# Kernel optimization log

Measured on AMD Instinct MI355X. Metric: run time of the kernel, lower is better.

Reference implementation:

```python
import jax, jax.numpy as jnp
import numpy as np

D_MODEL = 1024

def setup_inputs() -> dict:
    key = jax.random.key(0)
    ks = jax.random.split(key, 7)
    B, S, D = 4, 2048, D_MODEL
    scale = 1.0 / np.sqrt(D)
    x = jax.random.normal(ks[0], (B, S, D), dtype=jnp.float32)
    Wq = jax.random.normal(ks[1], (D, D), dtype=jnp.float32) * scale
    bq = jnp.zeros((D,), dtype=jnp.float32)
    Wk = jax.random.normal(ks[2], (D, D), dtype=jnp.float32) * scale
    bk = jnp.zeros((D,), dtype=jnp.float32)
    Wv = jax.random.normal(ks[3], (D, D), dtype=jnp.float32) * scale
    bv = jnp.zeros((D,), dtype=jnp.float32)
    return {"x": x, "Wq": Wq, "bq": bq, "Wk": Wk, "bk": bk, "Wv": Wv, "bv": bv}

def reference(x, Wq, bq, Wk, bk, Wv, bv):
    # Single-head attention; scale = 1/sqrt(d_model) as in the torch module (self.d_k = d_model).
    d_k = x.shape[-1]
    q = jnp.einsum('bsd,de->bse', x, Wq) + bq
    k = jnp.einsum('bsd,de->bse', x, Wk) + bk
    v = jnp.einsum('bsd,de->bse', x, Wv) + bv
    scores = jnp.einsum('bqd,bkd->bqk', q, k) / jnp.sqrt(jnp.asarray(d_k, x.dtype))
    attn = jax.nn.softmax(scores, axis=-1)
    return jnp.einsum('bqk,bkd->bqd', attn, v)
```

## Files before the change

### kernel.cpp

```cpp
#include <hip/hip_runtime.h>
#include <hip/hip_bf16.h>

#define DM 1024
#define SEQ 2048
#define NBATCH 4

using f32x4 = __attribute__((ext_vector_type(4))) float;
using s16x8 = __attribute__((ext_vector_type(8))) short;
using u16x4 = __attribute__((ext_vector_type(4))) unsigned short;
using u16x8 = __attribute__((ext_vector_type(8))) unsigned short;

__device__ __forceinline__ unsigned short f2bf(float f) {
  union { float f; unsigned u; } v; v.f = f;
  return (unsigned short)((v.u + 0x7fffu + ((v.u >> 16) & 1u)) >> 16);
}

__global__ void prep_k(const float* __restrict__ X,
                       const float* __restrict__ Wq, const float* __restrict__ Wk,
                       const float* __restrict__ Wv,
                       unsigned short* __restrict__ XB, unsigned short* __restrict__ WT) {
  __shared__ float t[32][33];
  const int b = blockIdx.x;
  if (b < 4096) {
    const int i = b * 256 + threadIdx.x;
    const f32x4* p = (const f32x4*)X;
    f32x4 a = p[2 * i], c = p[2 * i + 1];
    u16x8 o;
#pragma unroll
    for (int q = 0; q < 4; q++) { o[q] = f2bf(a[q]); o[4 + q] = f2bf(c[q]); }
    *(u16x8*)(XB + (size_t)i * 8) = o;
  } else {
    const int r2 = b - 4096;
    const int seg = r2 >> 10;
    const int rem = r2 & 1023;
    const int k0 = (rem >> 5) * 32, n0 = (rem & 31) * 32;
    const float* W = (seg == 0) ? Wq : (seg == 1) ? Wk : Wv;
    unsigned short* out = WT + (size_t)seg * DM * DM;
    const int tr = threadIdx.x >> 5, tc = threadIdx.x & 31;
#pragma unroll
    for (int p = 0; p < 4; p++) {
      int r = tr + p * 8;
      t[r][tc] = W[(size_t)(k0 + r) * DM + n0 + tc];
    }
    __syncthreads();
#pragma unroll
    for (int p = 0; p < 4; p++) {
      int r = tr + p * 8;
      out[(size_t)(n0 + r) * DM + k0 + tc] = f2bf(t[tc][r]);
    }
  }
}

__global__ void combine_k(const float* __restrict__ ms, const float* __restrict__ ss,
                          float* __restrict__ T) {
  const int idx = blockIdx.x * 256 + threadIdx.x;
  const float* m = ms + (size_t)idx * 16;
  const float* s = ss + (size_t)idx * 32;
  float mv[16];
#pragma unroll
  for (int t = 0; t < 16; t++) mv[t] = m[t];
  float M = mv[0];
#pragma unroll
  for (int t = 1; t < 16; t++) M = fmaxf(M, mv[t]);
  float L = 0.f;
#pragma unroll
  for (int t = 0; t < 16; t++) L += (s[2 * t] + s[2 * t + 1]) * __expf(mv[t] - M);
  T[idx] = 1.0f;
#pragma unroll
  for (int t = 1; t < 16; t++) T[t * 8192 + idx] = __expf(mv[t - 1] - mv[t]);
  T[16 * 8192 + idx] = __expf(mv[15] - M) / L;
}

template <int MODE, int LDA, int LDB, int KDIM>
__global__ void gemm_nt(const unsigned short* __restrict__ A,
                        const unsigned short* __restrict__ B,
                        void* __restrict__ C0,
                        unsigned short* __restrict__ C1,
                        unsigned short* __restrict__ C2,
                        const float* __restrict__ bq,
                        const float* __restrict__ bk,
                        const float* __restrict__ bv,
                        float* __restrict__ sm,
                        float* __restrict__ sv,
                        const float* __restrict__ Tt) {
  __shared__ unsigned short lbuf[16384];
  unsigned short* lA = lbuf;
  unsigned short* lB = lbuf + 8192;

  const int tid = threadIdx.x;
  const int w = tid >> 6;
  const int L = tid & 63;
  const int wm = w & 1, wn = w >> 1;
  const int qd = L >> 4, ll = L & 15;

  const int bid = blockIdx.x;
  const int xcd = bid & 7, slot = bid >> 3;
  int bz, tileM, tileN, nT;
  if (MODE == 0) {
    const int pm = xcd & 3, pn = xcd >> 2;
    const int nloc = slot % 12, mloc = slot / 12;
    bz = 0; tileM = (pm * 16 + mloc) * 128; tileN = (pn * 12 + nloc) * 128; nT = 0;
  } else if (MODE == 1) {
    bz = xcd >> 1;
    const int mh = xcd & 1;
    const int nloc = slot & 15, mloc = slot >> 4;
    tileM = (mh * 8 + mloc) * 128; tileN = nloc * 128; nT = nloc;
  } else {
    bz = xcd >> 1;
    const int mh = xcd & 1;
    const int nloc = slot & 7, mloc = slot >> 3;
    tileM = (mh * 8 + mloc) * 128; tileN = nloc * 128; nT = nloc;
  }

  const unsigned short* Ab = A;
  const unsigned short* Bb = B;
  if (MODE == 1) { Ab += (size_t)bz * SEQ * DM; Bb += (size_t)bz * SEQ * DM; }
  if (MODE == 2) { Ab += (size_t)bz * SEQ * SEQ; Bb += (size_t)bz * DM * SEQ; }

  const int srow = tid >> 3;
  const int pch = tid & 7;
  const int gch = pch ^ (srow & 7);
  const unsigned short* gA = Ab + (size_t)(tileM + srow) * LDA + gch * 8;
  const unsigned short* gB = Bb + (size_t)(tileN + srow) * LDB + gch * 8;
  unsigned short* wA = &lA[srow * 64 + pch * 8];
  unsigned short* wB = &lB[srow * 64 + pch * 8];

  u16x8 rA[4], rB[4];
#define LOADT(kt) do {                                                         \
    const size_t kk_ = (size_t)(kt) * 64;                                      \
    _Pragma("unroll")                                                          \
    for (int i_ = 0; i_ < 4; i_++) {                                           \
      rA[i_] = *(const u16x8*)(gA + (size_t)i_ * 32 * LDA + kk_);              \
      rB[i_] = *(const u16x8*)(gB + (size_t)i_ * 32 * LDB + kk_);              \
    }                                                                          \
  } while (0)
#define WRITET() do {                                                          \
    _Pragma("unroll")                                                          \
    for (int i_ = 0; i_ < 4; i_++) {                                           \
      *(u16x8*)(wA + i_ * 32 * 64) = rA[i_];                                   \
      *(u16x8*)(wB + i_ * 32 * 64) = rB[i_];                                   \
    }                                                                          \
  } while (0)

  f32x4 acc[4][4];
#pragma unroll
  for (int i = 0; i < 4; i++)
#pragma unroll
    for (int j = 0; j < 4; j++) acc[i][j] = (f32x4){0.f, 0.f, 0.f, 0.f};

  const int sw = L & 7;

  float tTn[4][4];
  const float* Tb = nullptr;
  if (MODE == 2) {
    Tb = Tt + (size_t)bz * SEQ + tileM + wm * 64;
#pragma unroll
    for (int i = 0; i < 4; i++)
#pragma unroll
      for (int r = 0; r < 4; r++) tTn[i][r] = Tb[1 * 8192 + i * 16 + qd * 4 + r];
  }

  constexpr int NK = KDIM / 64;
  LOADT(0);
  WRITET();
  __syncthreads();

  for (int k = 0; k < NK; ++k) {
    if (MODE == 2 && k >= 2 && (k & 1) == 0) {
#pragma unroll
      for (int i = 0; i < 4; i++)
#pragma unroll
        for (int j = 0; j < 4; j++)
#pragma unroll
          for (int r = 0; r < 4; r++) acc[i][j][r] *= tTn[i][r];
      const int tn = (k >> 1) + 1;
#pragma unroll
      for (int i = 0; i < 4; i++)
#pragma unroll
        for (int r = 0; r < 4; r++) tTn[i][r] = Tb[(size_t)tn * 8192 + i * 16 + qd * 4 + r];
    }

    if (k + 1 < NK) LOADT(k + 1);

#pragma unroll
    for (int s = 0; s < 2; s++) {
      const int pc = ((s * 4 + qd) ^ sw) * 8;
      s16x8 av[4], bv4[4];
#pragma unroll
      for (int i = 0; i < 4; i++)
        av[i] = *(const s16x8*)&lA[(wm * 64 + i * 16 + ll) * 64 + pc];
#pragma unroll
      for (int j = 0; j < 4; j++)
        bv4[j] = *(const s16x8*)&lB[(wn * 64 + j * 16 + ll) * 64 + pc];
#pragma unroll
      for (int i = 0; i < 4; i++)
#pragma unroll
        for (int j = 0; j < 4; j++)
          acc[i][j] = __builtin_amdgcn_mfma_f32_16x16x32_bf16(av[i], bv4[j], acc[i][j], 0, 0, 0);
    }

    if (k + 1 < NK) {
      __builtin_amdgcn_s_waitcnt(0xC07F);
      __builtin_amdgcn_sched_barrier(0);
      __builtin_amdgcn_s_barrier();
      __builtin_amdgcn_sched_barrier(0);
      WRITET();
      __syncthreads();
    }
  }
#undef LOADT
#undef WRITET

  if (MODE == 0) {
#pragma unroll
    for (int i = 0; i < 4; i++) {
      const int gm0 = tileM + wm * 64 + i * 16 + qd * 4;
#pragma unroll
      for (int j = 0; j < 4; j++) {
        const int gn = tileN + wn * 64 + j * 16 + ll;
        const int seg = gn >> 10;
        const int colin = gn & 1023;
        if (seg == 0) {
          const float bias = bq[colin];
          unsigned short* Q = (unsigned short*)C0;
#pragma unroll
          for (int r = 0; r < 4; r++) Q[(size_t)(gm0 + r) * DM + colin] = f2bf(acc[i][j][r] + bias);
        } else if (seg == 1) {
          const float bias = bk[colin];
#pragma unroll
          for (int r = 0; r < 4; r++) C1[(size_t)(gm0 + r) * DM + colin] = f2bf(acc[i][j][r] + bias);
        } else {
          const float bias = bv[colin];
          u16x4 pk;
#pragma unroll
          for (int r = 0; r < 4; r++) pk[r] = f2bf(acc[i][j][r] + bias);
          const int b = gm0 >> 11, s0 = gm0 & 2047;
          *(u16x4*)(C2 + ((size_t)((b << 10) + colin)) * SEQ + s0) = pk;
        }
      }
    }
  } else if (MODE == 1) {
    __syncthreads();
    float mt[4][4];
#pragma unroll
    for (int i = 0; i < 4; i++)
#pragma unroll
      for (int r = 0; r < 4; r++) {
#pragma unroll
        for (int j = 0; j < 4; j++) acc[i][j][r] *= 0.03125f;
        float v = fmaxf(fmaxf(acc[i][0][r], acc[i][1][r]), fmaxf(acc[i][2][r], acc[i][3][r]));
#pragma unroll
        for (int m = 1; m < 16; m <<= 1) v = fmaxf(v, __shfl_xor(v, m, 16));
        mt[i][r] = v;
      }
    float* fred = (float*)lbuf;
    if (ll == 0) {
#pragma unroll
      for (int i = 0; i < 4; i++)
#pragma unroll
        for (int r = 0; r < 4; r++)
          fred[wn * 128 + wm * 64 + i * 16 + qd * 4 + r] = mt[i][r];
    }
    __syncthreads();
#pragma unroll
    for (int i = 0; i < 4; i++)
#pragma unroll
      for (int r = 0; r < 4; r++) {
        const int row = wm * 64 + i * 16 + qd * 4 + r;
        mt[i][r] = fmaxf(fred[row], fred[128 + row]);
      }
    __syncthreads();
#pragma unroll
    for (int i = 0; i < 4; i++)
#pragma unroll
      for (int r = 0; r < 4; r++) {
        const int row = wm * 64 + i * 16 + qd * 4 + r;
        float s = 0.f;
#pragma unroll
        for (int j = 0; j < 4; j++) {
          float e = __expf(acc[i][j][r] - mt[i][r]);
          s += e;
          const int col = wn * 64 + j * 16 + ll;
          lbuf[row * 128 + ((((col >> 4) ^ (row & 7)) << 4) | (col & 15))] = f2bf(e);
        }
#pragma unroll
        for (int m = 1; m < 16; m <<= 1) s += __shfl_xor(s, m, 16);
        if (ll == 0) {
          const size_t base = (size_t)bz * SEQ + tileM + row;
          sv[base * 32 + nT * 2 + wn] = s;
          if (wn == 0) sm[base * 16 + nT] = mt[i][r];
        }
      }
    __syncthreads();
    unsigned short* P = (unsigned short*)C0 + (size_t)bz * SEQ * SEQ;
#pragma unroll
    for (int p = 0; p < 8; p++) {
      const int c = p * 256 + tid;
      const int row = c >> 4, cg = c & 15;
      const int phys = ((((cg >> 1) ^ (row & 7)) << 4) | ((cg & 1) << 3));
      u16x8 val = *(const u16x8*)&lbuf[row * 128 + phys];
      *(u16x8*)(P + (size_t)(tileM + row) * SEQ + tileN + cg * 8) = val;
    }
  } else {
    float* O = (float*)C0 + (size_t)bz * SEQ * DM;
#pragma unroll
    for (int i = 0; i < 4; i++) {
      const int gm0 = tileM + wm * 64 + i * 16 + qd * 4;
#pragma unroll
      for (int j = 0; j < 4; j++) {
        const int gn = tileN + wn * 64 + j * 16 + ll;
#pragma unroll
        for (int r = 0; r < 4; r++)
          O[(size_t)(gm0 + r) * DM + gn] = acc[i][j][r] * tTn[i][r];
      }
    }
  }
}

extern "C" void kernel_launch(void* const* d_in, const int* in_sizes, int n_in,
                              void* d_out, int out_size, void* d_ws, size_t ws_size,
                              hipStream_t stream) {
  (void)in_sizes; (void)n_in; (void)out_size; (void)ws_size;
  const float* x  = (const float*)d_in[0];
  const float* Wq = (const float*)d_in[1];
  const float* bq = (const float*)d_in[2];
  const float* Wk = (const float*)d_in[3];
  const float* bk = (const float*)d_in[4];
  const float* Wv = (const float*)d_in[5];
  const float* bv = (const float*)d_in[6];
  float* out = (float*)d_out;
  char* ws = (char*)d_ws;
  unsigned short* xb = (unsigned short*)(ws + 0);
  unsigned short* wt = (unsigned short*)(ws + 16777216);
  unsigned short* qb = (unsigned short*)(ws + 23068672);
  unsigned short* kb = (unsigned short*)(ws + 39845888);
  unsigned short* vt = (unsigned short*)(ws + 56623104);
  unsigned short* P  = (unsigned short*)(ws + 73400320);
  float*          ms = (float*)(ws + 106954752);
  float*          ss = (float*)(ws + 107479040);
  float*          Tt = (float*)(ws + 108527616);

  prep_k<<<7168, 256, 0, stream>>>(x, Wq, Wk, Wv, xb, wt);
  gemm_nt<0, 1024, 1024, 1024><<<1536, 256, 0, stream>>>(
      xb, wt, (void*)qb, kb, vt, bq, bk, bv, nullptr, nullptr, nullptr);
  gemm_nt<1, 1024, 1024, 1024><<<1024, 256, 0, stream>>>(
      qb, kb, (void*)P, nullptr, nullptr, nullptr, nullptr, nullptr, ms, ss, nullptr);
  combine_k<<<32, 256, 0, stream>>>(ms, ss, Tt);
  gemm_nt<2, 2048, 2048, 2048><<<512, 256, 0, stream>>>(
      P, vt, (void*)out, nullptr, nullptr, nullptr, nullptr, nullptr, nullptr, nullptr, Tt);
}
```

Measured before the change: 273.1 us.

## Double-buffer LDS tiles in GEMM with one barrier per k-step

The GEMM kernel gets two LDS buffers instead of one, and global loads are prefetched two k-tiles ahead into registers. Each iteration writes the next tile into the idle buffer before computing on the current one. This replaces the two barriers per iteration (one before and one after the LDS write) with a single barrier. The cost is doubling shared memory per block to 64 KB, which may reduce how many blocks fit on a CU.

```diff
diff --git a/kernel.cpp b/kernel.cpp
--- a/kernel.cpp
+++ b/kernel.cpp
@@ -83,9 +83,7 @@
                         float* __restrict__ sm,
                         float* __restrict__ sv,
                         const float* __restrict__ Tt) {
-  __shared__ unsigned short lbuf[16384];
-  unsigned short* lA = lbuf;
-  unsigned short* lB = lbuf + 8192;
+  __shared__ unsigned short lbuf[32768];
 
   const int tid = threadIdx.x;
   const int w = tid >> 6;
@@ -122,8 +120,8 @@
   const int gch = pch ^ (srow & 7);
   const unsigned short* gA = Ab + (size_t)(tileM + srow) * LDA + gch * 8;
   const unsigned short* gB = Bb + (size_t)(tileN + srow) * LDB + gch * 8;
-  unsigned short* wA = &lA[srow * 64 + pch * 8];
-  unsigned short* wB = &lB[srow * 64 + pch * 8];
+  unsigned short* wA0 = &lbuf[srow * 64 + pch * 8];
+  unsigned short* wB0 = wA0 + 8192;
 
   u16x8 rA[4], rB[4];
 #define LOADT(kt) do {                                                         \
@@ -134,12 +132,20 @@
       rB[i_] = *(const u16x8*)(gB + (size_t)i_ * 32 * LDB + kk_);              \
     }                                                                          \
   } while (0)
-#define WRITET() do {                                                          \
+#define WRITET(b) do {                                                         \
+    unsigned short* wa_ = wA0 + (b) * 16384;                                   \
+    unsigned short* wb_ = wB0 + (b) * 16384;                                   \
     _Pragma("unroll")                                                          \
     for (int i_ = 0; i_ < 4; i_++) {                                           \
-      *(u16x8*)(wA + i_ * 32 * 64) = rA[i_];                                   \
-      *(u16x8*)(wB + i_ * 32 * 64) = rB[i_];                                   \
+      *(u16x8*)(wa_ + i_ * 32 * 64) = rA[i_];                                  \
+      *(u16x8*)(wb_ + i_ * 32 * 64) = rB[i_];                                  \
     }                                                                          \
+  } while (0)
+#define RAWBAR() do {                                                          \
+    __builtin_amdgcn_s_waitcnt(0xC07F);                   \
+    __builtin_amdgcn_sched_barrier(0);                                         \
+    __builtin_amdgcn_s_barrier();                                              \
+    __builtin_amdgcn_sched_barrier(0);                                         \
   } while (0)
 
   f32x4 acc[4][4];
@@ -162,10 +168,13 @@
 
   constexpr int NK = KDIM / 64;
   LOADT(0);
-  WRITET();
-  __syncthreads();
+  WRITET(0);
+  LOADT(1);
+  RAWBAR();
 
   for (int k = 0; k < NK; ++k) {
+    if (k + 1 < NK) WRITET((k + 1) & 1);
+
     if (MODE == 2 && k >= 2 && (k & 1) == 0) {
 #pragma unroll
       for (int i = 0; i < 4; i++)
@@ -180,18 +189,20 @@
         for (int r = 0; r < 4; r++) tTn[i][r] = Tb[(size_t)tn * 8192 + i * 16 + qd * 4 + r];
     }
 
-    if (k + 1 < NK) LOADT(k + 1);
-
+    if (k + 2 < NK) LOADT(k + 2);
+
+    const unsigned short* cA = lbuf + (k & 1) * 16384;
+    const unsigned short* cB = cA + 8192;
 #pragma unroll
     for (int s = 0; s < 2; s++) {
       const int pc = ((s * 4 + qd) ^ sw) * 8;
       s16x8 av[4], bv4[4];
 #pragma unroll
       for (int i = 0; i < 4; i++)
-        av[i] = *(const s16x8*)&lA[(wm * 64 + i * 16 + ll) * 64 + pc];
+        av[i] = *(const s16x8*)&cA[(wm * 64 + i * 16 + ll) * 64 + pc];
 #pragma unroll
       for (int j = 0; j < 4; j++)
-        bv4[j] = *(const s16x8*)&lB[(wn * 64 + j * 16 + ll) * 64 + pc];
+        bv4[j] = *(const s16x8*)&cB[(wn * 64 + j * 16 + ll) * 64 + pc];
 #pragma unroll
       for (int i = 0; i < 4; i++)
 #pragma unroll
@@ -199,17 +210,11 @@
           acc[i][j] = __builtin_amdgcn_mfma_f32_16x16x32_bf16(av[i], bv4[j], acc[i][j], 0, 0, 0);
     }
 
-    if (k + 1 < NK) {
-      __builtin_amdgcn_s_waitcnt(0xC07F);
-      __builtin_amdgcn_sched_barrier(0);
-      __builtin_amdgcn_s_barrier();
-      __builtin_amdgcn_sched_barrier(0);
-      WRITET();
-      __syncthreads();
-    }
+    RAWBAR();
   }
 #undef LOADT
 #undef WRITET
+#undef RAWBAR
 
   if (MODE == 0) {
 #pragma unroll
```

Result: slower. 374.1 us (+37.0%).
